# Performance work log

Measured on AMD Instinct MI355X. Metric: run time of the kernel, lower is better.

## Reference

```python
import jax, jax.numpy as jnp
import numpy as np


def setup_inputs() -> dict:
    key = jax.random.key(0)
    k1, k2 = jax.random.split(key)
    visual_features = jax.random.normal(k1, (16, 1024, 768), dtype=jnp.float32)
    text_tokens = jax.random.normal(k2, (16, 256, 768), dtype=jnp.float32)
    return {"visual_features": visual_features, "text_tokens": text_tokens, "k": 16}


def reference(visual_features, text_tokens, k):
    B, N, D = visual_features.shape
    T = min(k, N)

    # normalize (note: norm + 1e-6 in denominator, matching torch code)
    vis_norm = visual_features / (jnp.linalg.norm(visual_features, axis=-1, keepdims=True) + 1e-6)
    vis_norm = vis_norm.astype(jnp.float32)
    txt_norm = text_tokens / (jnp.linalg.norm(text_tokens, axis=-1, keepdims=True) + 1e-6)
    txt_norm = txt_norm.astype(jnp.float32)

    similarity = jnp.einsum('bnd,bmd->bnm', vis_norm, vis_norm)          # (B,N,N)
    relevance = jnp.einsum('bnd,btd->bnt', vis_norm, txt_norm).max(-1)    # (B,N)
    r_min = relevance.min(axis=1, keepdims=True)
    r_max = relevance.max(axis=1, keepdims=True)
    relevance = (relevance - r_min + 1e-6) / (r_max - r_min + 1e-6)

    kernel = relevance[:, :, None] * similarity * relevance[:, None, :]   # (B,N,N)

    di2s0 = jnp.diagonal(kernel, axis1=1, axis2=2)                        # (B,N)
    cis0 = jnp.zeros((T, B, N), dtype=kernel.dtype)
    barange = jnp.arange(B)

    def step(carry, i):
        di2s, cis = carry
        safe = jnp.maximum(di2s, 1e-12)
        j = jnp.argmax(safe, axis=-1)                                     # (B,)
        k_j = jnp.take_along_axis(kernel, j[:, None, None], axis=1)[:, 0, :]  # (B,N)
        dj = jnp.take_along_axis(di2s, j[:, None], axis=1)[:, 0]          # (B,)
        denom = jnp.sqrt(jnp.maximum(dj, 1e-12))[:, None] + 1e-8          # (B,1)
        # cis rows >= i are zero, so full-T contraction equals contraction over :i
        c_tb = jnp.take_along_axis(cis, j[None, :, None], axis=2)[:, :, 0]  # (T,B)
        cov = jnp.einsum('tb,tbn->bn', c_tb, cis)                         # (B,N)
        eis = (k_j - cov) / denom                                         # (B,N)
        cis = jax.lax.dynamic_update_index_in_dim(cis, eis, i, axis=0)
        di2s = di2s - eis ** 2
        di2s = di2s.at[barange, j].set(-jnp.inf)
        return (di2s, cis), j

    (_, _), sel = jax.lax.scan(step, (di2s0, cis0), jnp.arange(T))        # sel: (T,B)
    select_idx = jnp.sort(sel.T, axis=1)                                  # (B,T)
    selected = jnp.take_along_axis(visual_features, select_idx[:, :, None], axis=1)  # (B,T,D)
    if T < k:
        pad = jnp.zeros((B, k - T, D), dtype=selected.dtype)
        selected = jnp.concatenate([selected, pad], axis=1)
    return selected
```

## Files before the change

kernel.cpp:

```cpp
#include <hip/hip_runtime.h>
#include <math.h>

#define NB 16
#define NN 1024
#define ND 768
#define NT 256
#define NSEL 16
#define NC 64

typedef __attribute__((ext_vector_type(8))) short short8;
typedef __attribute__((ext_vector_type(4))) float f32x4;
typedef __attribute__((ext_vector_type(8))) unsigned short ushort8v;
typedef unsigned long long u64;

__device__ __align__(16) float g_invv[NB*NN];
__device__ __align__(16) float g_diagv[NB*NN];
__device__ __align__(16) float g_mrawp[NB*NN*2];
__device__ __align__(16) ushort8v g_tf[NB*2*24*2*8*64];

__device__ __forceinline__ unsigned short f2bf(float x) {
    unsigned u = __float_as_uint(x);
    return (unsigned short)((u + 0x7FFFu + ((u >> 16) & 1u)) >> 16);
}
__device__ __forceinline__ float bf2f(unsigned short h) {
    return __uint_as_float(((unsigned)h) << 16);
}
__device__ __forceinline__ size_t tfidx(int b, int th, int s, int h, int ct, int lane) {
    return ((((size_t)(b*2 + th)*24 + s)*2 + h)*8 + ct)*64 + lane;
}

__global__ __launch_bounds__(256) void ktxt(const float* __restrict__ txt) {
    int gw = (blockIdx.x * 256 + threadIdx.x) >> 6;
    int l  = threadIdx.x & 63;
    int b  = gw >> 8, r = gw & 255;
    int th = r >> 7, ct = (r >> 4) & 7, rlo = r & 15;
    const float* row = txt + (size_t)gw * ND;

    float4 x0 = *(const float4*)(row + 8*l);
    float4 y0 = *(const float4*)(row + 8*l + 4);
    float4 x1 = {0,0,0,0}, y1 = {0,0,0,0};
    bool two = (l < 32);
    if (two) {
        x1 = *(const float4*)(row + 512 + 8*l);
        y1 = *(const float4*)(row + 512 + 8*l + 4);
    }
    float s = x0.x*x0.x + x0.y*x0.y + x0.z*x0.z + x0.w*x0.w
            + y0.x*y0.x + y0.y*y0.y + y0.z*y0.z + y0.w*y0.w;
    if (two) s += x1.x*x1.x + x1.y*x1.y + x1.z*x1.z + x1.w*x1.w
                + y1.x*y1.x + y1.y*y1.y + y1.z*y1.z + y1.w*y1.w;
    #pragma unroll
    for (int off = 32; off; off >>= 1) s += __shfl_xor(s, off);
    float inv = 1.0f / (sqrtf(s) + 1e-6f);

    int kslot = l & 3;
    int lane  = kslot*16 + rlo;
    {
        int st = l >> 2;
        float a[8] = {x0.x, x0.y, x0.z, x0.w, y0.x, y0.y, y0.z, y0.w};
        ushort8v hh, ll;
        #pragma unroll
        for (int j = 0; j < 8; j++) {
            float v = a[j] * inv;
            hh[j] = f2bf(v);
            ll[j] = f2bf(v - bf2f(hh[j]));
        }
        g_tf[tfidx(b, th, st, 0, ct, lane)] = hh;
        g_tf[tfidx(b, th, st, 1, ct, lane)] = ll;
    }
    if (two) {
        int st = 16 + (l >> 2);
        float a[8] = {x1.x, x1.y, x1.z, x1.w, y1.x, y1.y, y1.z, y1.w};
        ushort8v hh, ll;
        #pragma unroll
        for (int j = 0; j < 8; j++) {
            float v = a[j] * inv;
            hh[j] = f2bf(v);
            ll[j] = f2bf(v - bf2f(hh[j]));
        }
        g_tf[tfidx(b, th, st, 0, ct, lane)] = hh;
        g_tf[tfidx(b, th, st, 1, ct, lane)] = ll;
    }
}

__global__ __launch_bounds__(256) void krel(const float* __restrict__ vis) {
    int bid = blockIdx.x;
    int lid = (bid & 7) * 64 + (bid >> 3);
    int b   = lid >> 5;
    int mt  = (lid >> 1) & 15;
    int th  = lid & 1;
    int t   = threadIdx.x;
    int w   = t >> 6, l = t & 63;

    __shared__ __align__(16) ushort8v Bfrag[3][2][8][64];

    f32x4 acc[8];
    #pragma unroll
    for (int ct = 0; ct < 8; ct++) acc[ct] = (f32x4){0.f, 0.f, 0.f, 0.f};

    int arow = mt*64 + w*16 + (l & 15);
    const float* Ap = vis + ((size_t)(b*NN + arow))*ND + (l >> 4)*8;

    const ushort8v* Bbase = g_tf + tfidx(b, th, 0, 0, 0, 0);

    #define STAGE(S, P)                                                          \
        {                                                                        \
            _Pragma("unroll")                                                    \
            for (int q = 0; q < 4; q++) {                                        \
                int c  = w*4 + q;                                                \
                int h  = c >> 3, ct = c & 7;                                     \
                const ushort8v* gsrc = Bbase + (((size_t)(S)*2 + h)*8 + ct)*64 + l; \
                __builtin_amdgcn_global_load_lds(                                \
                    (const __attribute__((address_space(1))) void*)gsrc,         \
                    (__attribute__((address_space(3))) void*)&Bfrag[P][h][ct][0],\
                    16, 0, 0);                                                   \
            }                                                                    \
        }

    #define CONV(AX, AY, AH, AL, SS)                                             \
        {                                                                        \
            float av_[8] = {AX.x, AX.y, AX.z, AX.w, AY.x, AY.y, AY.z, AY.w};     \
            ushort8v hh_, ll_;                                                   \
            _Pragma("unroll")                                                    \
            for (int j = 0; j < 8; j++) {                                        \
                hh_[j] = f2bf(av_[j]);                                           \
                ll_[j] = f2bf(av_[j] - bf2f(hh_[j]));                            \
                SS = fmaf(av_[j], av_[j], SS);                                   \
            }                                                                    \
            AH = *(short8*)&hh_;                                                 \
            AL = *(short8*)&ll_;                                                 \
        }

    float4 rax = *(const float4*)(Ap);
    float4 ray = *(const float4*)(Ap + 4);
    STAGE(0, 0);
    STAGE(1, 1);
    float ss = 0.f;
    short8 ah, al;
    CONV(rax, ray, ah, al, ss);
    rax = *(const float4*)(Ap + 32);
    ray = *(const float4*)(Ap + 36);
    __syncthreads();

    for (int s = 0; s < 24; s++) {
        int p = s % 3;
        if (s < 22) STAGE(s + 2, (s + 2) % 3);
        asm volatile("" ::: "memory");
        short8 ahn, aln;
        if (s < 23) CONV(rax, ray, ahn, aln, ss);
        if (s < 22) {
            rax = *(const float4*)(Ap + (s + 2) * 32);
            ray = *(const float4*)(Ap + (s + 2) * 32 + 4);
        }
        #pragma unroll
        for (int ct = 0; ct < 8; ct++) {
            short8 bh = *(const short8*)&Bfrag[p][0][ct][l];
            short8 bl = *(const short8*)&Bfrag[p][1][ct][l];
            acc[ct] = __builtin_amdgcn_mfma_f32_16x16x32_bf16(ah, bh, acc[ct], 0, 0, 0);
            acc[ct] = __builtin_amdgcn_mfma_f32_16x16x32_bf16(al, bh, acc[ct], 0, 0, 0);
            acc[ct] = __builtin_amdgcn_mfma_f32_16x16x32_bf16(ah, bl, acc[ct], 0, 0, 0);
            acc[ct] = __builtin_amdgcn_mfma_f32_16x16x32_bf16(al, bl, acc[ct], 0, 0, 0);
        }
        if (s < 23) { ah = ahn; al = aln; }
        if (s < 23) {
            asm volatile("s_waitcnt lgkmcnt(0)" ::: "memory");
            __builtin_amdgcn_s_barrier();
            __builtin_amdgcn_sched_barrier(0);
        }
    }
    #undef STAGE
    #undef CONV

    #pragma unroll
    for (int r = 0; r < 4; r++) {
        float m = acc[0][r];
        #pragma unroll
        for (int ct = 1; ct < 8; ct++) m = fmaxf(m, acc[ct][r]);
        #pragma unroll
        for (int off = 1; off <= 8; off <<= 1) m = fmaxf(m, __shfl_xor(m, off));
        if ((l & 15) == 0)
            g_mrawp[(size_t)(b*NN + mt*64 + w*16 + (l >> 4)*4 + r)*2 + th] = m;
    }

    ss += __shfl_xor(ss, 16);
    ss += __shfl_xor(ss, 32);
    if (th == 0 && l < 16) {
        int row = mt*64 + w*16 + l;
        float nrm = sqrtf(ss);
        float inv = 1.0f / (nrm + 1e-6f);
        g_invv[b*NN + row] = inv;
        float dd = nrm * inv;
        g_diagv[b*NN + row] = dd * dd;
    }
}

__global__ __launch_bounds__(1024) void kfinal(const float* __restrict__ vis,
                                               float* __restrict__ out) {
    int b = blockIdx.x;
    int t = threadIdx.x;
    int w = t >> 6, l = t & 63;

    __shared__ u64   s_key[NN];
    __shared__ float s_reln[NN];
    __shared__ __align__(16) unsigned short Chi[NC][392], Clo[NC][392];
    __shared__ float s_S[NC*65];
    __shared__ int   s_sel[NSEL], s_srt[NSEL];
    __shared__ float s_mn[16], s_mx[16], s_b2[2];

    float m0 = g_mrawp[(size_t)(b*NN + t)*2 + 0];
    float m1 = g_mrawp[(size_t)(b*NN + t)*2 + 1];
    float iv = g_invv[b*NN + t], dd = g_diagv[b*NN + t];
    float rr = fmaxf(m0, m1) * iv;
    float lmin = rr, lmax = rr;
    #pragma unroll
    for (int off = 32; off; off >>= 1) {
        lmin = fminf(lmin, __shfl_xor(lmin, off));
        lmax = fmaxf(lmax, __shfl_xor(lmax, off));
    }
    if (l == 0) { s_mn[w] = lmin; s_mx[w] = lmax; }
    __syncthreads();
    if (t == 0) {
        float mn = s_mn[0], mx = s_mx[0];
        #pragma unroll
        for (int q = 1; q < 16; q++) { mn = fminf(mn, s_mn[q]); mx = fmaxf(mx, s_mx[q]); }
        s_b2[0] = mn; s_b2[1] = mx;
    }
    __syncthreads();
    float mn = s_b2[0], mx = s_b2[1];
    float den = mx - mn + 1e-6f;
    float rn = (rr - mn + 1e-6f) / den;
    float d0 = rn * rn * dd;
    s_reln[t] = rn;
    u64 kreg = ((u64)(~__float_as_uint(d0)) << 10) | (unsigned)t;

    #pragma unroll
    for (int k = 2; k <= 64; k <<= 1) {
        #pragma unroll
        for (int j = k >> 1; j > 0; j >>= 1) {
            u64 part = __shfl_xor(kreg, j);
            bool takeMin = ((l & k) == 0) == ((l & j) == 0);
            kreg = takeMin ? (kreg < part ? kreg : part) : (kreg < part ? part : kreg);
        }
    }
    #pragma unroll
    for (int rnd = 0; rnd < 4; rnd++) {
        int dstp = 8 >> rnd;
        s_key[w*64 + l] = kreg;
        __syncthreads();
        u64 other = s_key[(w ^ dstp)*64 + (63 - l)];
        u64 m = (kreg < other) ? kreg : other;
        #pragma unroll
        for (int j = 32; j > 0; j >>= 1) {
            u64 part = __shfl_xor(m, j);
            bool takeMin = ((l & j) == 0);
            m = takeMin ? (m < part ? m : part) : (m < part ? part : m);
        }
        kreg = m;
        __syncthreads();
    }

    int   gid = (int)(kreg & 1023u);
    float d0v = __uint_as_float(~(unsigned)(kreg >> 10));

    f32x4 acc = (f32x4){0.f, 0.f, 0.f, 0.f};
    int ar0 = (w >> 2) * 16, bc0 = (w & 3) * 16;
    int cr  = (w << 2) + (l >> 4);
    int sgid = __shfl(gid, cr);
    float sc = g_invv[b*NN + sgid];
    const float* srcrow = vis + (size_t)(b*NN + sgid)*ND + (l & 15)*24;

    for (int c = 0; c < 2; c++) {
        __syncthreads();
        int kb = (l & 15) * 24;
        #pragma unroll
        for (int q = 0; q < 3; q++) {
            float4 x = *(const float4*)(srcrow + c*384 + q*8);
            float4 y = *(const float4*)(srcrow + c*384 + q*8 + 4);
            float av[8] = {x.x, x.y, x.z, x.w, y.x, y.y, y.z, y.w};
            ushort8v hh, ll;
            #pragma unroll
            for (int j = 0; j < 8; j++) {
                float vv = av[j] * sc;
                hh[j] = f2bf(vv);
                ll[j] = f2bf(vv - bf2f(hh[j]));
            }
            *(ushort8v*)&Chi[cr][kb + q*8] = hh;
            *(ushort8v*)&Clo[cr][kb + q*8] = ll;
        }
        __syncthreads();
        #pragma unroll
        for (int ks = 0; ks < 12; ks++) {
            int ko = ks*32 + (l >> 4)*8;
            short8 ah = *(const short8*)&Chi[ar0 + (l & 15)][ko];
            short8 al = *(const short8*)&Clo[ar0 + (l & 15)][ko];
            short8 bh = *(const short8*)&Chi[bc0 + (l & 15)][ko];
            short8 bl = *(const short8*)&Clo[bc0 + (l & 15)][ko];
            acc = __builtin_amdgcn_mfma_f32_16x16x32_bf16(ah, bh, acc, 0, 0, 0);
            acc = __builtin_amdgcn_mfma_f32_16x16x32_bf16(al, bh, acc, 0, 0, 0);
            acc = __builtin_amdgcn_mfma_f32_16x16x32_bf16(ah, bl, acc, 0, 0, 0);
            acc = __builtin_amdgcn_mfma_f32_16x16x32_bf16(al, bl, acc, 0, 0, 0);
        }
    }
    #pragma unroll
    for (int r = 0; r < 4; r++)
        s_S[(ar0 + (l >> 4)*4 + r)*65 + bc0 + (l & 15)] = acc[r];
    __syncthreads();

    if (w == 0) {
        float di  = d0v;
        int   gd  = gid;
        float rel = s_reln[gid];
        float ownc[NSEL];
        #pragma unroll
        for (int i = 0; i < NSEL; i++) {
            float vq = fmaxf(di, 1e-12f);
            int   gq = gd;
            int   cq = l;
            #pragma unroll
            for (int off = 32; off; off >>= 1) {
                float vo = __shfl_xor(vq, off);
                int   go = __shfl_xor(gq, off);
                int   co = __shfl_xor(cq, off);
                if (vo > vq || (vo == vq && go < gq)) { vq = vo; gq = go; cq = co; }
            }
            float dj   = __shfl(di, cq);
            float relj = __shfl(rel, cq);
            float denom = sqrtf(fmaxf(dj, 1e-12f)) + 1e-8f;
            if (l == 0) s_sel[i] = gq;

            float cov = 0.f;
            #pragma unroll
            for (int q = 0; q < i; q++)
                cov = fmaf(ownc[q], __shfl(ownc[q], cq), cov);

            float sim = s_S[l*65 + cq];
            float kj  = rel * relj * sim;
            float eis = (kj - cov) / denom;
            ownc[i] = eis;
            di = di - eis * eis;
            if (l == cq) di = -__builtin_inff();
        }
    }
    __syncthreads();

    if (t == 0) {
        int vv[16];
        #pragma unroll
        for (int q = 0; q < 16; q++) vv[q] = s_sel[q];
        for (int a = 1; a < 16; a++) {
            int key = vv[a]; int p2 = a - 1;
            while (p2 >= 0 && vv[p2] > key) { vv[p2+1] = vv[p2]; p2--; }
            vv[p2+1] = key;
        }
        #pragma unroll
        for (int q = 0; q < 16; q++) s_srt[q] = vv[q];
    }
    __syncthreads();
    {
        int idx = s_srt[w];
        const float* src = vis + (size_t)(b*NN + idx)*ND + l*12;
        float*       dst = out + (size_t)(b*NSEL + w)*ND + l*12;
        float4 x = *(const float4*)(src);
        float4 y = *(const float4*)(src + 4);
        float4 z = *(const float4*)(src + 8);
        *(float4*)(dst)     = x;
        *(float4*)(dst + 4) = y;
        *(float4*)(dst + 8) = z;
    }
}

extern "C" void kernel_launch(void* const* d_in, const int* in_sizes, int n_in,
                              void* d_out, int out_size, void* d_ws, size_t ws_size,
                              hipStream_t stream) {
    (void)in_sizes; (void)n_in; (void)d_ws; (void)ws_size; (void)out_size;
    const float* vis = (const float*)d_in[0];
    const float* txt = (const float*)d_in[1];
    float* out = (float*)d_out;

    ktxt  <<<dim3((NB*NT)/4), dim3(256),  0, stream>>>(txt);
    krel  <<<dim3(512),       dim3(256),  0, stream>>>(vis);
    kfinal<<<dim3(NB),        dim3(1024), 0, stream>>>(vis, out);
}
```

Baseline: 73.50 us.

## Drop lo*lo MFMA term and restructure relevance GEMM to double-buffered 64-wide k-steps

Removes the low-times-low bf16 MFMA product in both the relevance GEMM and the similarity GEMM, cutting split-precision MFMA work from four products to three per step. The krel main loop moves from a triple-buffered 32-wide k pipeline to a double-buffered 64-wide one, with half as many barriers, an explicit vmcnt wait, and A-operand prefetch one step ahead. The dropped term is second-order, so accuracy should stay near fp32, but the small extra error could flip argmax ties in the greedy selection.

```diff
diff --git a/kernel.cpp b/kernel.cpp
--- a/kernel.cpp
+++ b/kernel.cpp
@@ -91,27 +91,28 @@
     int t   = threadIdx.x;
     int w   = t >> 6, l = t & 63;
 
-    __shared__ __align__(16) ushort8v Bfrag[3][2][8][64];
+    __shared__ __align__(16) ushort8v Bfrag[2][2][2][8][64];
 
     f32x4 acc[8];
     #pragma unroll
     for (int ct = 0; ct < 8; ct++) acc[ct] = (f32x4){0.f, 0.f, 0.f, 0.f};
 
     int arow = mt*64 + w*16 + (l & 15);
-    const float* Ap = vis + ((size_t)(b*NN + arow))*ND + (l >> 4)*8;
+    int akq  = (l >> 4) * 8;
+    const float* Ap = vis + ((size_t)(b*NN + arow))*ND + akq;
 
     const ushort8v* Bbase = g_tf + tfidx(b, th, 0, 0, 0, 0);
 
     #define STAGE(S, P)                                                          \
         {                                                                        \
             _Pragma("unroll")                                                    \
-            for (int q = 0; q < 4; q++) {                                        \
-                int c  = w*4 + q;                                                \
-                int h  = c >> 3, ct = c & 7;                                     \
-                const ushort8v* gsrc = Bbase + (((size_t)(S)*2 + h)*8 + ct)*64 + l; \
+            for (int q = 0; q < 8; q++) {                                        \
+                int c   = w*8 + q;                                               \
+                int sub = c >> 4, h = (c >> 3) & 1, ct = c & 7;                  \
+                const ushort8v* gsrc = Bbase + (((size_t)((S)*2 + sub)*2 + h)*8 + ct)*64 + l; \
                 __builtin_amdgcn_global_load_lds(                                \
                     (const __attribute__((address_space(1))) void*)gsrc,         \
-                    (__attribute__((address_space(3))) void*)&Bfrag[P][h][ct][0],\
+                    (__attribute__((address_space(3))) void*)&Bfrag[P][sub][h][ct][0],\
                     16, 0, 0);                                                   \
             }                                                                    \
         }
@@ -130,39 +131,48 @@
             AL = *(short8*)&ll_;                                                 \
         }
 
-    float4 rax = *(const float4*)(Ap);
-    float4 ray = *(const float4*)(Ap + 4);
+    float4 a0x = *(const float4*)(Ap);
+    float4 a0y = *(const float4*)(Ap + 4);
+    float4 a1x = *(const float4*)(Ap + 32);
+    float4 a1y = *(const float4*)(Ap + 36);
     STAGE(0, 0);
-    STAGE(1, 1);
+    __syncthreads();
     float ss = 0.f;
-    short8 ah, al;
-    CONV(rax, ray, ah, al, ss);
-    rax = *(const float4*)(Ap + 32);
-    ray = *(const float4*)(Ap + 36);
-    __syncthreads();
-
-    for (int s = 0; s < 24; s++) {
-        int p = s % 3;
-        if (s < 22) STAGE(s + 2, (s + 2) % 3);
+
+    for (int S = 0; S < 12; S++) {
+        int p = S & 1;
+        if (S < 11) STAGE(S + 1, (S + 1) & 1);
         asm volatile("" ::: "memory");
-        short8 ahn, aln;
-        if (s < 23) CONV(rax, ray, ahn, aln, ss);
-        if (s < 22) {
-            rax = *(const float4*)(Ap + (s + 2) * 32);
-            ray = *(const float4*)(Ap + (s + 2) * 32 + 4);
-        }
+        float4 n0x, n0y, n1x, n1y;
+        if (S < 11) {
+            int k1 = (S + 1) * 64;
+            n0x = *(const float4*)(Ap + k1);
+            n0y = *(const float4*)(Ap + k1 + 4);
+            n1x = *(const float4*)(Ap + k1 + 32);
+            n1y = *(const float4*)(Ap + k1 + 36);
+        }
+        short8 ah0, al0, ah1, al1;
+        CONV(a0x, a0y, ah0, al0, ss);
+        CONV(a1x, a1y, ah1, al1, ss);
         #pragma unroll
         for (int ct = 0; ct < 8; ct++) {
-            short8 bh = *(const short8*)&Bfrag[p][0][ct][l];
-            short8 bl = *(const short8*)&Bfrag[p][1][ct][l];
-            acc[ct] = __builtin_amdgcn_mfma_f32_16x16x32_bf16(ah, bh, acc[ct], 0, 0, 0);
-            acc[ct] = __builtin_amdgcn_mfma_f32_16x16x32_bf16(al, bh, acc[ct], 0, 0, 0);
-            acc[ct] = __builtin_amdgcn_mfma_f32_16x16x32_bf16(ah, bl, acc[ct], 0, 0, 0);
-            acc[ct] = __builtin_amdgcn_mfma_f32_16x16x32_bf16(al, bl, acc[ct], 0, 0, 0);
-        }
-        if (s < 23) { ah = ahn; al = aln; }
-        if (s < 23) {
-            asm volatile("s_waitcnt lgkmcnt(0)" ::: "memory");
+            short8 bh = *(const short8*)&Bfrag[p][0][0][ct][l];
+            short8 bl = *(const short8*)&Bfrag[p][0][1][ct][l];
+            acc[ct] = __builtin_amdgcn_mfma_f32_16x16x32_bf16(ah0, bh, acc[ct], 0, 0, 0);
+            acc[ct] = __builtin_amdgcn_mfma_f32_16x16x32_bf16(al0, bh, acc[ct], 0, 0, 0);
+            acc[ct] = __builtin_amdgcn_mfma_f32_16x16x32_bf16(ah0, bl, acc[ct], 0, 0, 0);
+        }
+        #pragma unroll
+        for (int ct = 0; ct < 8; ct++) {
+            short8 bh = *(const short8*)&Bfrag[p][1][0][ct][l];
+            short8 bl = *(const short8*)&Bfrag[p][1][1][ct][l];
+            acc[ct] = __builtin_amdgcn_mfma_f32_16x16x32_bf16(ah1, bh, acc[ct], 0, 0, 0);
+            acc[ct] = __builtin_amdgcn_mfma_f32_16x16x32_bf16(al1, bh, acc[ct], 0, 0, 0);
+            acc[ct] = __builtin_amdgcn_mfma_f32_16x16x32_bf16(ah1, bl, acc[ct], 0, 0, 0);
+        }
+        if (S < 11) { a0x = n0x; a0y = n0y; a1x = n1x; a1y = n1y; }
+        if (S < 11) {
+            asm volatile("s_waitcnt vmcnt(4) lgkmcnt(0)" ::: "memory");
             __builtin_amdgcn_s_barrier();
             __builtin_amdgcn_sched_barrier(0);
         }
@@ -297,7 +307,6 @@
             acc = __builtin_amdgcn_mfma_f32_16x16x32_bf16(ah, bh, acc, 0, 0, 0);
             acc = __builtin_amdgcn_mfma_f32_16x16x32_bf16(al, bh, acc, 0, 0, 0);
             acc = __builtin_amdgcn_mfma_f32_16x16x32_bf16(ah, bl, acc, 0, 0, 0);
-            acc = __builtin_amdgcn_mfma_f32_16x16x32_bf16(al, bl, acc, 0, 0, 0);
         }
     }
     #pragma unroll
```

After: 68.94 us (median of 2 runs). -6.2%, faster.
